# Kernel optimization log

Measured on AMD Instinct MI355X. Metric: run time of the kernel, lower is better.

The kernel has to match this reference:

```python
import jax, jax.numpy as jnp
import numpy as np

B, N, A, IN_DIM, OUT_DIM, D_OBS = 4096, 16, 8, 128, 128, 128


def setup_inputs() -> dict:
    key = jax.random.key(0)
    k1, k2, k3, k4, k5, k6 = jax.random.split(key, 6)
    h = jax.random.normal(k1, (B, N, IN_DIM), dtype=jnp.float32)
    policies = jax.random.uniform(k2, (B, N, A), dtype=jnp.float32)
    actions = jax.random.uniform(k3, (B, N, A), dtype=jnp.float32)
    obs_proc = jax.random.normal(k4, (B * N, D_OBS), dtype=jnp.float32)
    # xavier-normal-ish params (exact init values irrelevant for correctness baseline)
    W_fc = jax.random.normal(k5, (OUT_DIM, IN_DIM), dtype=jnp.float32) * (2.0 / (IN_DIM + OUT_DIM)) ** 0.5
    W_attn = jax.random.normal(k6, (1, 2 * OUT_DIM), dtype=jnp.float32) * (2.0 / (2 * OUT_DIM + 1)) ** 0.5
    return {"h": h, "policies": policies, "actions": actions, "obs_proc": obs_proc,
            "W_fc": W_fc, "W_attn": W_attn}


def reference(h, policies, actions, obs_proc, W_fc, W_attn):
    # h: [B, N, in_dim]; policies/actions: [B, N, A]; obs_proc: [B*N, D]
    b, n, a = policies.shape
    z = jnp.einsum('bni,oi->bno', h, W_fc)                    # fc(h), [B, N, out]
    out_dim = z.shape[-1]
    # attn_fc(cat[z_src, z_dst]) split into src/dst contributions
    a_src = z @ W_attn[0, :out_dim]                           # [B, N]
    a_dst = z @ W_attn[0, out_dim:]                           # [B, N]
    # e[b, i(dst), j(src)] = leaky_relu(a_src[b,j] + a_dst[b,i])
    e = jax.nn.leaky_relu(a_src[:, None, :] + a_dst[:, :, None], 0.01)
    w = jax.nn.sigmoid(e)[..., None]                          # [B, N(dst), N(src), 1]
    # gated mix of source action / source policy per (dst, src) pair
    zgate = w * actions[:, None, :, :] + (1.0 - w) * policies[:, None, :, :]  # [B,i,j,A]
    # repeat + place_policies/place_zs masked sum + mean over src dim collapses to:
    # out_z[b,i,k] = (sum_j zgate[b,i,j] - zgate[b,i,k] + policies[b,k]) / N
    sum_z = zgate.sum(axis=2)                                 # [B, i, A]
    out_z = (sum_z[:, :, None, :] - zgate + policies[:, None, :, :]) / n  # [B,i,k,A]
    obs_b = obs_proc.reshape(b, n, -1)                        # [B, k, D]
    d = obs_b.shape[-1]
    obs_rep = jnp.broadcast_to(obs_b[:, None, :, :], (b, n, n, d))  # [B, i, k, D]
    obs_final = jnp.concatenate([obs_rep, out_z], axis=-1).reshape(b * n, n, d + a)
    return obs_final, w.reshape(b * n, n, 1)
```

## Files before the change

### kernel.cpp

```cpp
#include <hip/hip_runtime.h>
#include <math.h>

#define B_SZ 4096
#define N_SZ 16
#define A_SZ 8
#define IN_DIM 128
#define OUT_DIM 128
#define D_OBS 128
#define ROW_OUT (D_OBS + A_SZ)

typedef float f32x4 __attribute__((ext_vector_type(4)));

__global__ __launch_bounds__(1024) void prep_v(const float* __restrict__ W_fc,
                                               const float* __restrict__ W_attn,
                                               float* __restrict__ v) {
  __shared__ float part[8][2][128];
  const int i = threadIdx.x & 127;
  const int seg = threadIdx.x >> 7;
  float s = 0.f, d = 0.f;
  #pragma unroll
  for (int oo = 0; oo < 16; ++oo) {
    const int o = seg * 16 + oo;
    const float w = W_fc[o * IN_DIM + i];
    s += w * W_attn[o];
    d += w * W_attn[OUT_DIM + o];
  }
  part[seg][0][i] = s;
  part[seg][1][i] = d;
  __syncthreads();
  if (seg == 0) {
    float ss = 0.f, dd = 0.f;
    #pragma unroll
    for (int t = 0; t < 8; ++t) { ss += part[t][0][i]; dd += part[t][1][i]; }
    v[i] = ss;
    v[IN_DIM + i] = dd;
  }
}

__global__ __launch_bounds__(256) void gat_main(
    const float* __restrict__ h,
    const float* __restrict__ pol,
    const float* __restrict__ act,
    const float* __restrict__ obs,
    const float* __restrict__ v,
    float* __restrict__ out_obs,
    float* __restrict__ out_w)
{
  const int b = ((blockIdx.x & 7) << 9) | (blockIdx.x >> 3);
  const int tid = threadIdx.x;

  __shared__ float a_src_sm[16];
  __shared__ float a_dst_sm[16];
  __shared__ float w_sm[256];
  __shared__ float pol_sm[128];
  __shared__ float act_sm[128];
  __shared__ float sumz_sm[128];
  __shared__ float outz_sm[2048];
  __shared__ float obs_sm[2048];

  {
    const f32x4* op = (const f32x4*)(obs + (size_t)b * (N_SZ * D_OBS));
    f32x4* od = (f32x4*)obs_sm;
    od[tid]       = __builtin_nontemporal_load(&op[tid]);
    od[tid + 256] = __builtin_nontemporal_load(&op[tid + 256]);
  }
  if (tid < 128) {
    pol_sm[tid] = __builtin_nontemporal_load(&pol[(size_t)b * (N_SZ * A_SZ) + tid]);
    act_sm[tid] = __builtin_nontemporal_load(&act[(size_t)b * (N_SZ * A_SZ) + tid]);
  }

  {
    const int l = tid & 15;
    const f32x4* hp = (const f32x4*)(h + (size_t)b * (N_SZ * IN_DIM));
    const f32x4 h0 = __builtin_nontemporal_load(&hp[tid * 2]);
    const f32x4 h1 = __builtin_nontemporal_load(&hp[tid * 2 + 1]);
    const f32x4* vs = (const f32x4*)v;
    const f32x4* vd = (const f32x4*)(v + IN_DIM);
    const f32x4 s0 = vs[l * 2], s1 = vs[l * 2 + 1];
    const f32x4 d0 = vd[l * 2], d1 = vd[l * 2 + 1];
    float s = h0.x * s0.x + h0.y * s0.y + h0.z * s0.z + h0.w * s0.w
            + h1.x * s1.x + h1.y * s1.y + h1.z * s1.z + h1.w * s1.w;
    float d = h0.x * d0.x + h0.y * d0.y + h0.z * d0.z + h0.w * d0.w
            + h1.x * d1.x + h1.y * d1.y + h1.z * d1.z + h1.w * d1.w;
    for (int m = 8; m >= 1; m >>= 1) {
      s += __shfl_xor(s, m, 16);
      d += __shfl_xor(d, m, 16);
    }
    if (l == 0) {
      a_src_sm[tid >> 4] = s;
      a_dst_sm[tid >> 4] = d;
    }
  }
  __syncthreads();

  {
    float e = a_src_sm[tid & 15] + a_dst_sm[tid >> 4];
    e = (e >= 0.f) ? e : 0.01f * e;
    const float wv = 1.f / (1.f + expf(-e));
    w_sm[tid] = wv;
    out_w[(size_t)b * 256 + tid] = wv;
  }
  __syncthreads();

  if (tid < 128) {
    const int i = tid >> 3, a = tid & 7;
    float s = 0.f;
    #pragma unroll
    for (int j = 0; j < N_SZ; ++j) {
      const float wv = w_sm[i * 16 + j];
      s += wv * act_sm[j * 8 + a] + (1.f - wv) * pol_sm[j * 8 + a];
    }
    sumz_sm[tid] = s;
  }
  __syncthreads();

  {
    const int i = tid >> 4, k = tid & 15;
    const float wv = w_sm[tid];
    #pragma unroll
    for (int a = 0; a < A_SZ; ++a) {
      const float zg = wv * act_sm[k * 8 + a] + (1.f - wv) * pol_sm[k * 8 + a];
      outz_sm[tid * 8 + a] =
          (sumz_sm[i * 8 + a] - zg + pol_sm[k * 8 + a]) * 0.0625f;
    }
  }
  __syncthreads();

  float* ob = out_obs + (size_t)b * (256 * ROW_OUT);
  const f32x4* obs4 = (const f32x4*)obs_sm;
  {
    int r  = tid / 34;
    int d4 = tid - r * 34;
    #pragma unroll 2
    for (int idx = tid; idx < 256 * 34; idx += 256) {
      f32x4 o4;
      if (d4 < 32) {
        o4 = obs4[(r & 15) * 32 + d4];
      } else {
        o4 = *(const f32x4*)(outz_sm + r * 8 + (d4 - 32) * 4);
      }
      *(f32x4*)(ob + (size_t)idx * 4) = o4;
      r += 7; d4 += 18;
      if (d4 >= 34) { d4 -= 34; ++r; }
    }
  }
}

extern "C" void kernel_launch(void* const* d_in, const int* in_sizes, int n_in,
                              void* d_out, int out_size, void* d_ws, size_t ws_size,
                              hipStream_t stream) {
  const float* h      = (const float*)d_in[0];
  const float* pol    = (const float*)d_in[1];
  const float* act    = (const float*)d_in[2];
  const float* obs    = (const float*)d_in[3];
  const float* W_fc   = (const float*)d_in[4];
  const float* W_attn = (const float*)d_in[5];

  float* out = (float*)d_out;
  float* out_w = out + (size_t)B_SZ * N_SZ * N_SZ * ROW_OUT;
  float* v = (float*)d_ws;

  prep_v<<<1, 1024, 0, stream>>>(W_fc, W_attn, v);
  gat_main<<<B_SZ, 256, 0, stream>>>(h, pol, act, obs, v, out, out_w);
}
```

Before: 138.5 us.

## Split into compute kernel and grid-stride streaming writer with recomputed gates

Splits the per-batch kernel in two. A small compute kernel writes a_src, a_dst and the per-destination gate sums to workspace. A separate grid-stride streaming kernel then writes the large output with nontemporal stores, recomputing the sigmoid gate and out_z per element on the fly. The aim is to decouple the bandwidth-bound output write from the per-batch shared-memory staging and barriers and to give it full occupancy. In exchange it adds an extra launch, workspace round trips, a divide by 34 per element, and redundant gate recomputation. It falls back to the old kernel if the workspace is too small.

```diff
diff --git a/kernel.cpp b/kernel.cpp
--- a/kernel.cpp
+++ b/kernel.cpp
@@ -7,9 +7,15 @@
 #define IN_DIM 128
 #define OUT_DIM 128
 #define D_OBS 128
-#define ROW_OUT (D_OBS + A_SZ)
+#define ROW_OUT 136
 
 typedef float f32x4 __attribute__((ext_vector_type(4)));
+
+#define WS_V      0
+#define WS_ASRC   256
+#define WS_ADST   (256 + B_SZ * 16)
+#define WS_SUMZ   (256 + B_SZ * 32)
+#define WS_FLOATS (256 + B_SZ * 32 + B_SZ * 128)
 
 __global__ __launch_bounds__(1024) void prep_v(const float* __restrict__ W_fc,
                                                const float* __restrict__ W_attn,
@@ -37,36 +43,26 @@
   }
 }
 
-__global__ __launch_bounds__(256) void gat_main(
+__global__ __launch_bounds__(256) void gat_compute(
     const float* __restrict__ h,
     const float* __restrict__ pol,
     const float* __restrict__ act,
-    const float* __restrict__ obs,
-    const float* __restrict__ v,
-    float* __restrict__ out_obs,
+    float* __restrict__ ws,
     float* __restrict__ out_w)
 {
-  const int b = ((blockIdx.x & 7) << 9) | (blockIdx.x >> 3);
+  const int b = blockIdx.x;
   const int tid = threadIdx.x;
+  const float* v = ws + WS_V;
 
   __shared__ float a_src_sm[16];
   __shared__ float a_dst_sm[16];
   __shared__ float w_sm[256];
   __shared__ float pol_sm[128];
   __shared__ float act_sm[128];
-  __shared__ float sumz_sm[128];
-  __shared__ float outz_sm[2048];
-  __shared__ float obs_sm[2048];
-
-  {
-    const f32x4* op = (const f32x4*)(obs + (size_t)b * (N_SZ * D_OBS));
-    f32x4* od = (f32x4*)obs_sm;
-    od[tid]       = __builtin_nontemporal_load(&op[tid]);
-    od[tid + 256] = __builtin_nontemporal_load(&op[tid + 256]);
-  }
-  if (tid < 128) {
-    pol_sm[tid] = __builtin_nontemporal_load(&pol[(size_t)b * (N_SZ * A_SZ) + tid]);
-    act_sm[tid] = __builtin_nontemporal_load(&act[(size_t)b * (N_SZ * A_SZ) + tid]);
+
+  if (tid < 128) {
+    pol_sm[tid] = pol[(size_t)b * 128 + tid];
+    act_sm[tid] = act[(size_t)b * 128 + tid];
   }
 
   {
@@ -93,6 +89,9 @@
   }
   __syncthreads();
 
+  if (tid < 16)       ws[WS_ASRC + b * 16 + tid] = a_src_sm[tid];
+  else if (tid < 32)  ws[WS_ADST + b * 16 + (tid - 16)] = a_dst_sm[tid - 16];
+
   {
     float e = a_src_sm[tid & 15] + a_dst_sm[tid >> 4];
     e = (e >= 0.f) ? e : 0.01f * e;
@@ -110,10 +109,114 @@
       const float wv = w_sm[i * 16 + j];
       s += wv * act_sm[j * 8 + a] + (1.f - wv) * pol_sm[j * 8 + a];
     }
+    ws[WS_SUMZ + b * 128 + tid] = s;
+  }
+}
+
+__global__ __launch_bounds__(256) void gat_stream_full(
+    const float* __restrict__ obs,
+    const float* __restrict__ pol,
+    const float* __restrict__ act,
+    const float* __restrict__ ws,
+    float* __restrict__ out_obs)
+{
+  const float* __restrict__ asrc = ws + WS_ASRC;
+  const float* __restrict__ adst = ws + WS_ADST;
+  const f32x4* __restrict__ sumz4 = (const f32x4*)(ws + WS_SUMZ);
+  const f32x4* __restrict__ obs4 = (const f32x4*)obs;
+  const f32x4* __restrict__ pol4 = (const f32x4*)pol;
+  const f32x4* __restrict__ act4 = (const f32x4*)act;
+
+  const unsigned total = B_SZ * 256u * 34u;
+  const unsigned stride = gridDim.x * blockDim.x;
+  for (unsigned idx = blockIdx.x * blockDim.x + threadIdx.x;
+       idx < total; idx += stride) {
+    const unsigned r  = idx / 34u;
+    const unsigned d4 = idx - r * 34u;
+    const unsigned bk = ((r >> 8) << 4) | (r & 15u);
+    f32x4 val;
+    if (d4 < 32u) {
+      val = obs4[(size_t)bk * 32 + d4];
+    } else {
+      const unsigned t  = d4 - 32u;
+      const unsigned bi = ((r >> 8) << 4) | ((r >> 4) & 15u);
+      float e = asrc[bk] + adst[bi];
+      e = (e >= 0.f) ? e : 0.01f * e;
+      const float wv = 1.f / (1.f + expf(-e));
+      const f32x4 pv = pol4[bk * 2 + t];
+      const f32x4 av = act4[bk * 2 + t];
+      const f32x4 sv = sumz4[bi * 2 + t];
+      val = (sv - (wv * av + (1.f - wv) * pv) + pv) * 0.0625f;
+    }
+    __builtin_nontemporal_store(val, (f32x4*)out_obs + idx);
+  }
+}
+
+__global__ __launch_bounds__(256) void gat_main_old(
+    const float* __restrict__ h, const float* __restrict__ pol,
+    const float* __restrict__ act, const float* __restrict__ obs,
+    const float* __restrict__ v, float* __restrict__ out_obs,
+    float* __restrict__ out_w)
+{
+  const int b = ((blockIdx.x & 7) << 9) | (blockIdx.x >> 3);
+  const int tid = threadIdx.x;
+  __shared__ float a_src_sm[16];
+  __shared__ float a_dst_sm[16];
+  __shared__ float w_sm[256];
+  __shared__ float pol_sm[128];
+  __shared__ float act_sm[128];
+  __shared__ float sumz_sm[128];
+  __shared__ float outz_sm[2048];
+  __shared__ float obs_sm[2048];
+  {
+    const f32x4* op = (const f32x4*)(obs + (size_t)b * (N_SZ * D_OBS));
+    f32x4* od = (f32x4*)obs_sm;
+    od[tid]       = __builtin_nontemporal_load(&op[tid]);
+    od[tid + 256] = __builtin_nontemporal_load(&op[tid + 256]);
+  }
+  if (tid < 128) {
+    pol_sm[tid] = pol[(size_t)b * 128 + tid];
+    act_sm[tid] = act[(size_t)b * 128 + tid];
+  }
+  {
+    const int l = tid & 15;
+    const f32x4* hp = (const f32x4*)(h + (size_t)b * (N_SZ * IN_DIM));
+    const f32x4 h0 = __builtin_nontemporal_load(&hp[tid * 2]);
+    const f32x4 h1 = __builtin_nontemporal_load(&hp[tid * 2 + 1]);
+    const f32x4* vs = (const f32x4*)v;
+    const f32x4* vd = (const f32x4*)(v + IN_DIM);
+    const f32x4 s0 = vs[l * 2], s1 = vs[l * 2 + 1];
+    const f32x4 d0 = vd[l * 2], d1 = vd[l * 2 + 1];
+    float s = h0.x * s0.x + h0.y * s0.y + h0.z * s0.z + h0.w * s0.w
+            + h1.x * s1.x + h1.y * s1.y + h1.z * s1.z + h1.w * s1.w;
+    float d = h0.x * d0.x + h0.y * d0.y + h0.z * d0.z + h0.w * d0.w
+            + h1.x * d1.x + h1.y * d1.y + h1.z * d1.z + h1.w * d1.w;
+    for (int m = 8; m >= 1; m >>= 1) {
+      s += __shfl_xor(s, m, 16);
+      d += __shfl_xor(d, m, 16);
+    }
+    if (l == 0) { a_src_sm[tid >> 4] = s; a_dst_sm[tid >> 4] = d; }
+  }
+  __syncthreads();
+  {
+    float e = a_src_sm[tid & 15] + a_dst_sm[tid >> 4];
+    e = (e >= 0.f) ? e : 0.01f * e;
+    const float wv = 1.f / (1.f + expf(-e));
+    w_sm[tid] = wv;
+    out_w[(size_t)b * 256 + tid] = wv;
+  }
+  __syncthreads();
+  if (tid < 128) {
+    const int i = tid >> 3, a = tid & 7;
+    float s = 0.f;
+    #pragma unroll
+    for (int j = 0; j < N_SZ; ++j) {
+      const float wv = w_sm[i * 16 + j];
+      s += wv * act_sm[j * 8 + a] + (1.f - wv) * pol_sm[j * 8 + a];
+    }
     sumz_sm[tid] = s;
   }
   __syncthreads();
-
   {
     const int i = tid >> 4, k = tid & 15;
     const float wv = w_sm[tid];
@@ -125,7 +228,6 @@
     }
   }
   __syncthreads();
-
   float* ob = out_obs + (size_t)b * (256 * ROW_OUT);
   const f32x4* obs4 = (const f32x4*)obs_sm;
   {
@@ -158,8 +260,14 @@
 
   float* out = (float*)d_out;
   float* out_w = out + (size_t)B_SZ * N_SZ * N_SZ * ROW_OUT;
-  float* v = (float*)d_ws;
-
-  prep_v<<<1, 1024, 0, stream>>>(W_fc, W_attn, v);
-  gat_main<<<B_SZ, 256, 0, stream>>>(h, pol, act, obs, v, out, out_w);
-}
+  float* ws = (float*)d_ws;
+
+  prep_v<<<1, 1024, 0, stream>>>(W_fc, W_attn, ws + WS_V);
+
+  if (ws_size >= (size_t)WS_FLOATS * sizeof(float)) {
+    gat_compute<<<B_SZ, 256, 0, stream>>>(h, pol, act, ws, out_w);
+    gat_stream_full<<<2048, 256, 0, stream>>>(obs, pol, act, ws, out);
+  } else {
+    gat_main_old<<<B_SZ, 256, 0, stream>>>(h, pol, act, obs, ws + WS_V, out, out_w);
+  }
+}
```

New measurement: 152.9 us. 1.1x slower.
